# Kernel optimization log

Measured on AMD Instinct MI355X. Metric: run time of the kernel, lower is better.

Reference implementation:

```python
import jax, jax.numpy as jnp
import numpy as np

B, SQ, SK = 8, 2048, 2048
QE = KE = VE = HID = 1024
NORM = HID ** 0.5


def setup_inputs() -> dict:
    key0 = jax.random.key(0)
    ks = jax.random.split(key0, 9)
    s = 1.0 / np.sqrt(HID)
    return {
        "key": jax.random.normal(ks[0], (B, SK, KE), dtype=jnp.float32),
        "query": jax.random.normal(ks[1], (B, SQ, QE), dtype=jnp.float32),
        "mask": jax.random.randint(ks[2], (B, SQ, SK), 0, 2, dtype=jnp.int32),
        # nn.Linear params: W has shape [out, in], y = x @ W.T + b
        "Wq": jax.random.uniform(ks[3], (HID, QE), jnp.float32, -s, s),
        "bq": jax.random.uniform(ks[4], (HID,), jnp.float32, -s, s),
        "Wk": jax.random.uniform(ks[5], (HID, KE), jnp.float32, -s, s),
        "bk": jax.random.uniform(ks[6], (HID,), jnp.float32, -s, s),
        "Wv": jax.random.uniform(ks[7], (HID, VE), jnp.float32, -s, s),
        "bv": jax.random.uniform(ks[8], (HID,), jnp.float32, -s, s),
    }


def reference(key, query, mask, Wq, bq, Wk, bk, Wv, bv):
    # QKV projections (note: value projection is applied to `key`, as in the original)
    q = jnp.einsum('bse,he->bsh', query, Wq) + bq   # [B,SQ,H]
    k = jnp.einsum('bse,he->bsh', key, Wk) + bk     # [B,SK,H]
    v = jnp.einsum('bse,he->bsh', key, Wv) + bv     # [B,SK,H]
    # scores + mask (0 -> -inf) in one fused pass
    score = jnp.einsum('bqh,bkh->bqk', q, k) / NORM  # [B,SQ,SK]
    score = jnp.where(mask == 0, -jnp.inf, score)
    score = jax.nn.softmax(score, axis=-1)
    # NaN cleanup for fully-masked rows (score.data[score != score] = 0)
    score = jnp.where(jnp.isnan(score), 0.0, score)
    output = jnp.einsum('bqk,bkh->bqh', score, v)    # [B,SQ,H]
    return (output, score)
```

## Files before the change

### kernel.cpp

```cpp
#include <hip/hip_runtime.h>
#include <hip/hip_bf16.h>

typedef __bf16 bf16;
typedef __bf16 bf16x8 __attribute__((ext_vector_type(8)));
typedef float  f32x4  __attribute__((ext_vector_type(4)));
typedef int    i32x4  __attribute__((ext_vector_type(4)));

#define TM 128
#define TN 128
#define TK 32
#define LDS_PAD 40

typedef __attribute__((address_space(3))) void       lds_t;
typedef __attribute__((address_space(1))) const void gbl_t;
__device__ __forceinline__ void async16(const void* g, void* l) {
    __builtin_amdgcn_global_load_lds((gbl_t*)g, (lds_t*)l, 16, 0, 0);
}

template<typename TC, int BIAS, int NTC>
__global__ __launch_bounds__(256)
void gemm_bt(const bf16* __restrict__ A, const bf16* __restrict__ B,
             TC* __restrict__ C, const float* __restrict__ bias,
             int K, int lda, int ldb, int ldc,
             long sA, long sB, long sC)
{
    constexpr int ASZ = TM * TK;
    constexpr int BSZ = TN * TK;
    constexpr int BUF = ASZ + BSZ;
    __shared__ bf16 lds[3 * BUF];

    const int gx = gridDim.x, gy = gridDim.y;
    int lin = blockIdx.x + gx * (blockIdx.y + gy * blockIdx.z);
    const int cpx = (gx * gy * gridDim.z) >> 3;
    lin = (lin & 7) * cpx + (lin >> 3);
    const int bx  = lin % gx;
    const int rem = lin / gx;
    const int by  = rem % gy;
    const int bz  = rem / gy;

    A += (long)bz * sA;  B += (long)bz * sB;  C += (long)bz * sC;

    const int m0 = by * TM;
    const int n0 = bx * TN;

    const int t    = threadIdx.x;
    const int lane = t & 63;
    const int wave = t >> 6;
    const int wm   = (wave >> 1) * 64;
    const int wn   = (wave & 1) * 64;
    const int lrow = lane & 15;
    const int quad = lane >> 4;

    const int srow = lane >> 2;
    const int scol = (lane & 3) * 8;

    const bf16* pA = &A[(long)(m0 + wave * 16 + srow) * lda + scol];
    const bf16* pB = &B[(long)(n0 + wave * 16 + srow) * ldb + scol];
    const long jA = (long)64 * lda;
    const long jB = (long)64 * ldb;

    const int NT_ = K / TK;

    auto stage = [&](int tile, int oS) {
        const int k0 = tile * TK;
        #pragma unroll
        for (int j = 0; j < 2; ++j) {
            const int rg = j * 64 + wave * 16;
            async16(pA + j * jA + k0, &lds[oS + rg * TK]);
            async16(pB + j * jB + k0, &lds[oS + ASZ + rg * TK]);
        }
    };

    stage(0, 0);
    asm volatile("" ::: "memory");
    stage(1, BUF);

    int oC = 0, oN = BUF, oS = 2 * BUF;
    f32x4 acc[4][4] = {};

    for (int tt = 0; tt < NT_; ++tt) {
        if (tt < NT_ - 1) asm volatile("s_waitcnt vmcnt(4) lgkmcnt(0)" ::: "memory");
        else              asm volatile("s_waitcnt vmcnt(0) lgkmcnt(0)" ::: "memory");
        __builtin_amdgcn_s_barrier();
        __builtin_amdgcn_sched_barrier(0);

        if (tt + 2 < NT_) stage(tt + 2, oS);

        bf16x8 af[4], bfr[4];
        #pragma unroll
        for (int i = 0; i < 4; ++i)
            af[i] = *(bf16x8*)&lds[oC + (wm + i * 16 + lrow) * TK + quad * 8];
        #pragma unroll
        for (int j = 0; j < 4; ++j)
            bfr[j] = *(bf16x8*)&lds[oC + ASZ + (wn + j * 16 + lrow) * TK + quad * 8];

        #pragma unroll
        for (int i = 0; i < 4; ++i)
            #pragma unroll
            for (int j = 0; j < 4; ++j)
                acc[i][j] = __builtin_amdgcn_mfma_f32_16x16x32_bf16(
                    af[i], bfr[j], acc[i][j], 0, 0, 0);

        const int tmp = oC; oC = oN; oN = oS; oS = tmp;
    }

    #pragma unroll
    for (int i = 0; i < 4; ++i) {
        #pragma unroll
        for (int j = 0; j < 4; ++j) {
            #pragma unroll
            for (int r = 0; r < 4; ++r) {
                const int row = m0 + wm + i * 16 + quad * 4 + r;
                const int col = n0 + wn + j * 16 + lrow;
                float v = acc[i][j][r];
                if (BIAS == 1) v += bias[col];
                if (BIAS == 2) v += bias[row];
                if constexpr (NTC)
                    __builtin_nontemporal_store((TC)v, &C[(long)row * ldc + col]);
                else
                    C[(long)row * ldc + col] = (TC)v;
            }
        }
    }
}

__global__ __launch_bounds__(256)
void cvt_f32_bf16(const float* __restrict__ x, bf16* __restrict__ y)
{
    const long i = ((long)blockIdx.x * 256 + threadIdx.x) * 8;
    const f32x4 a = __builtin_nontemporal_load((const f32x4*)(x + i));
    const f32x4 b = __builtin_nontemporal_load((const f32x4*)(x + i + 4));
    bf16x8 v;
    v[0] = (bf16)a[0]; v[1] = (bf16)a[1]; v[2] = (bf16)a[2]; v[3] = (bf16)a[3];
    v[4] = (bf16)b[0]; v[5] = (bf16)b[1]; v[6] = (bf16)b[2]; v[7] = (bf16)b[3];
    *(bf16x8*)(y + i) = v;
}

template<typename T>
__device__ inline void stage8(bf16* dst, const T* src) {
    if constexpr (sizeof(T) == 4) {
        const float4 f0 = *(const float4*)src;
        const float4 f1 = *(const float4*)(src + 4);
        bf16x8 v;
        v[0] = (bf16)f0.x; v[1] = (bf16)f0.y; v[2] = (bf16)f0.z; v[3] = (bf16)f0.w;
        v[4] = (bf16)f1.x; v[5] = (bf16)f1.y; v[6] = (bf16)f1.z; v[7] = (bf16)f1.w;
        *(bf16x8*)dst = v;
    } else {
        *(uint4*)dst = *(const uint4*)src;
    }
}

template<typename TA, typename TB, typename TC, int BIAS>
__global__ __launch_bounds__(256)
void gemm_nt(const TA* __restrict__ A, const TB* __restrict__ B,
             TC* __restrict__ C, const float* __restrict__ bias,
             int K, int lda, int ldb, int ldc,
             long sA, long sB, long sC)
{
    __shared__ bf16 lsA[TM * LDS_PAD];
    __shared__ bf16 lsB[TN * LDS_PAD];

    const int bz = blockIdx.z;
    A += (long)bz * sA;  B += (long)bz * sB;  C += (long)bz * sC;

    const int m0 = blockIdx.y * TM;
    const int n0 = blockIdx.x * TN;

    const int t    = threadIdx.x;
    const int lane = t & 63;
    const int wave = t >> 6;
    const int wm   = (wave >> 1) * 64;
    const int wn   = (wave & 1) * 64;
    const int lrow = lane & 15;
    const int quad = lane >> 4;
    const int sr = t >> 2;
    const int sk = (t & 3) * 8;

    f32x4 acc[4][4] = {};

    for (int k0 = 0; k0 < K; k0 += TK) {
        __syncthreads();
        #pragma unroll
        for (int h = 0; h < 2; ++h) {
            const int row = h * 64 + sr;
            stage8(&lsA[row * LDS_PAD + sk], &A[(long)(m0 + row) * lda + k0 + sk]);
            stage8(&lsB[row * LDS_PAD + sk], &B[(long)(n0 + row) * ldb + k0 + sk]);
        }
        __syncthreads();

        bf16x8 af[4], bfr[4];
        #pragma unroll
        for (int i = 0; i < 4; ++i)
            af[i] = *(bf16x8*)&lsA[(wm + i * 16 + lrow) * LDS_PAD + quad * 8];
        #pragma unroll
        for (int j = 0; j < 4; ++j)
            bfr[j] = *(bf16x8*)&lsB[(wn + j * 16 + lrow) * LDS_PAD + quad * 8];

        #pragma unroll
        for (int i = 0; i < 4; ++i)
            #pragma unroll
            for (int j = 0; j < 4; ++j)
                acc[i][j] = __builtin_amdgcn_mfma_f32_16x16x32_bf16(
                    af[i], bfr[j], acc[i][j], 0, 0, 0);
    }

    #pragma unroll
    for (int i = 0; i < 4; ++i) {
        #pragma unroll
        for (int j = 0; j < 4; ++j) {
            #pragma unroll
            for (int r = 0; r < 4; ++r) {
                const int row = m0 + wm + i * 16 + quad * 4 + r;
                const int col = n0 + wn + j * 16 + lrow;
                float v = acc[i][j][r];
                if (BIAS == 1) v += bias[col];
                if (BIAS == 2) v += bias[row];
                C[(long)row * ldc + col] = (TC)v;
            }
        }
    }
}

template<int DUAL>
__global__ __launch_bounds__(256)
void softmax_rows(float* __restrict__ score, const int* __restrict__ mask,
                  bf16* __restrict__ pb)
{
    const int t = threadIdx.x;
    const long base = (long)blockIdx.x * 2048 + t * 8;

    const f32x4 a0 = __builtin_nontemporal_load((const f32x4*)(score + base));
    const f32x4 a1 = __builtin_nontemporal_load((const f32x4*)(score + base + 4));
    const i32x4 mA = __builtin_nontemporal_load((const i32x4*)(mask + base));
    const i32x4 mB = __builtin_nontemporal_load((const i32x4*)(mask + base + 4));

    const float INV = 0.03125f;
    float s[8];
    #pragma unroll
    for (int i = 0; i < 4; ++i) s[i]     = mA[i] ? a0[i] * INV : -INFINITY;
    #pragma unroll
    for (int i = 0; i < 4; ++i) s[4 + i] = mB[i] ? a1[i] * INV : -INFINITY;

    float mx = s[0];
    #pragma unroll
    for (int i = 1; i < 8; ++i) mx = fmaxf(mx, s[i]);
    #pragma unroll
    for (int o = 32; o > 0; o >>= 1) mx = fmaxf(mx, __shfl_xor(mx, o, 64));

    __shared__ float redm[4], reds[4];
    const int wave = t >> 6, lane = t & 63;
    if (lane == 0) redm[wave] = mx;
    __syncthreads();
    mx = fmaxf(fmaxf(redm[0], redm[1]), fmaxf(redm[2], redm[3]));

    const bool dead = !(mx > -INFINITY);
    float e[8], sum = 0.f;
    #pragma unroll
    for (int i = 0; i < 8; ++i) {
        const float x = dead ? 0.0f : __expf(s[i] - mx);
        e[i] = x;
        sum += x;
    }
    #pragma unroll
    for (int o = 32; o > 0; o >>= 1) sum += __shfl_xor(sum, o, 64);
    if (lane == 0) reds[wave] = sum;
    __syncthreads();
    sum = reds[0] + reds[1] + reds[2] + reds[3];

    const float inv = dead ? 0.0f : (1.0f / sum);
    f32x4 o0, o1;
    float p[8];
    #pragma unroll
    for (int i = 0; i < 8; ++i) p[i] = e[i] * inv;
    o0[0] = p[0]; o0[1] = p[1]; o0[2] = p[2]; o0[3] = p[3];
    o1[0] = p[4]; o1[1] = p[5]; o1[2] = p[6]; o1[3] = p[7];

    __builtin_nontemporal_store(o0, (f32x4*)(score + base));
    __builtin_nontemporal_store(o1, (f32x4*)(score + base + 4));
    if (DUAL) {
        bf16x8 v;
        #pragma unroll
        for (int i = 0; i < 8; ++i) v[i] = (bf16)p[i];
        *(bf16x8*)(pb + base) = v;
    }
}

extern "C" void kernel_launch(void* const* d_in, const int* in_sizes, int n_in,
                              void* d_out, int out_size, void* d_ws, size_t ws_size,
                              hipStream_t stream)
{
    const float* key   = (const float*)d_in[0];
    const float* query = (const float*)d_in[1];
    const int*   mask  = (const int*)d_in[2];
    const float* Wq = (const float*)d_in[3];
    const float* bq = (const float*)d_in[4];
    const float* Wk = (const float*)d_in[5];
    const float* bk = (const float*)d_in[6];
    const float* Wv = (const float*)d_in[7];
    const float* bv = (const float*)d_in[8];

    float* out   = (float*)d_out;
    float* score = out + (size_t)8 * 2048 * 1024;

    const dim3 blk(256, 1, 1);
    const long SB = (long)2048 * 1024;
    const long SS = (long)2048 * 2048;
    const size_t NX = (size_t)8 * 2048 * 1024;
    const size_t NW = (size_t)1024 * 1024;

    const size_t NEED = (4 * NX + 3 * NW) * sizeof(bf16);

    if (ws_size >= NEED) {
        bf16* xb = (bf16*)d_ws;
        bf16* qb = xb + NX;
        bf16* kb = qb + NX;
        bf16* vt = kb + NX;
        bf16* wq = vt + NX;
        bf16* wk = wq + NW;
        bf16* wv = wk + NW;
        bf16* Pb = xb;

        cvt_f32_bf16<<<dim3(NW / 2048), blk, 0, stream>>>(Wq, wq);
        cvt_f32_bf16<<<dim3(NW / 2048), blk, 0, stream>>>(Wk, wk);
        cvt_f32_bf16<<<dim3(NW / 2048), blk, 0, stream>>>(Wv, wv);

        cvt_f32_bf16<<<dim3(NX / 2048), blk, 0, stream>>>(key, xb);
        gemm_bt<bf16, 1, 0><<<dim3(8, 128, 1), blk, 0, stream>>>(
            xb, wk, kb, bk, 1024, 1024, 1024, 1024, 0, 0, 0);
        gemm_bt<bf16, 2, 0><<<dim3(16, 8, 8), blk, 0, stream>>>(
            wv, xb, vt, bv, 1024, 1024, 1024, 2048, 0, SB, SB);

        cvt_f32_bf16<<<dim3(NX / 2048), blk, 0, stream>>>(query, xb);
        gemm_bt<bf16, 1, 0><<<dim3(8, 128, 1), blk, 0, stream>>>(
            xb, wq, qb, bq, 1024, 1024, 1024, 1024, 0, 0, 0);

        gemm_bt<float, 0, 1><<<dim3(16, 16, 8), blk, 0, stream>>>(
            qb, kb, score, nullptr, 1024, 1024, 1024, 2048, SB, SB, SS);

        softmax_rows<1><<<dim3(16384), blk, 0, stream>>>(score, mask, Pb);

        gemm_bt<float, 0, 1><<<dim3(8, 16, 8), blk, 0, stream>>>(
            Pb, vt, out, nullptr, 2048, 2048, 2048, 1024, SS, SB, SB);
    } else {
        bf16* qb = (bf16*)d_ws;
        bf16* kb = qb + NX;
        bf16* vt = kb + NX;

        gemm_nt<float, float, bf16, 1><<<dim3(8, 128, 1), blk, 0, stream>>>(
            query, Wq, qb, bq, 1024, 1024, 1024, 1024, 0, 0, 0);
        gemm_nt<float, float, bf16, 1><<<dim3(8, 128, 1), blk, 0, stream>>>(
            key, Wk, kb, bk, 1024, 1024, 1024, 1024, 0, 0, 0);
        gemm_nt<float, float, bf16, 2><<<dim3(16, 8, 8), blk, 0, stream>>>(
            Wv, key, vt, bv, 1024, 1024, 1024, 2048, 0, SB, SB);
        gemm_nt<bf16, bf16, float, 0><<<dim3(16, 16, 8), blk, 0, stream>>>(
            qb, kb, score, nullptr, 1024, 1024, 1024, 2048, SB, SB, SS);
        softmax_rows<0><<<dim3(16384), blk, 0, stream>>>(score, mask, nullptr);
        gemm_nt<float, bf16, float, 0><<<dim3(8, 16, 8), blk, 0, stream>>>(
            score, vt, out, nullptr, 2048, 2048, 2048, 1024, SS, SB, SB);
    }
}
```

Before: 686.8 us.

## Enlarge gemm_bt block tile to 256x128 and cache score between GEMM and softmax

The pipelined bf16 GEMM moves from a 128x128 to a 256x128 output tile per block. Each wave now computes 128x64 with an 8x4 accumulator array, so there are more MFMAs per LDS B-fragment and fewer blocks, and the grids are halved to match. Launch bounds request two blocks per CU. The score store is switched from nontemporal to normal stores and softmax loads it with plain loads, so the 128MB score buffer may partly stay in cache between the two kernels. The larger tile raises register and LDS pressure and halves the number of blocks, which could hurt occupancy.

```diff
diff --git a/kernel.cpp b/kernel.cpp
--- a/kernel.cpp
+++ b/kernel.cpp
@@ -6,9 +6,9 @@
 typedef float  f32x4  __attribute__((ext_vector_type(4)));
 typedef int    i32x4  __attribute__((ext_vector_type(4)));
 
-#define TM 128
-#define TN 128
 #define TK 32
+#define FB_TM 128
+#define FB_TN 128
 #define LDS_PAD 40
 
 typedef __attribute__((address_space(3))) void       lds_t;
@@ -18,16 +18,17 @@
 }
 
 template<typename TC, int BIAS, int NTC>
-__global__ __launch_bounds__(256)
+__global__ __launch_bounds__(256, 2)
 void gemm_bt(const bf16* __restrict__ A, const bf16* __restrict__ B,
              TC* __restrict__ C, const float* __restrict__ bias,
              int K, int lda, int ldb, int ldc,
              long sA, long sB, long sC)
 {
-    constexpr int ASZ = TM * TK;
-    constexpr int BSZ = TN * TK;
-    constexpr int BUF = ASZ + BSZ;
-    __shared__ bf16 lds[3 * BUF];
+    constexpr int BM  = 256, BN = 128;
+    constexpr int ASZ = BM * TK;
+    constexpr int BSZ = BN * TK;
+    constexpr int BUFE = ASZ + BSZ;
+    __shared__ bf16 lds[3 * BUFE];
 
     const int gx = gridDim.x, gy = gridDim.y;
     int lin = blockIdx.x + gx * (blockIdx.y + gy * blockIdx.z);
@@ -40,13 +41,13 @@
 
     A += (long)bz * sA;  B += (long)bz * sB;  C += (long)bz * sC;
 
-    const int m0 = by * TM;
-    const int n0 = bx * TN;
+    const int m0 = by * BM;
+    const int n0 = bx * BN;
 
     const int t    = threadIdx.x;
     const int lane = t & 63;
     const int wave = t >> 6;
-    const int wm   = (wave >> 1) * 64;
+    const int wm   = (wave >> 1) * 128;
     const int wn   = (wave & 1) * 64;
     const int lrow = lane & 15;
     const int quad = lane >> 4;
@@ -56,46 +57,46 @@
 
     const bf16* pA = &A[(long)(m0 + wave * 16 + srow) * lda + scol];
     const bf16* pB = &B[(long)(n0 + wave * 16 + srow) * ldb + scol];
-    const long jA = (long)64 * lda;
-    const long jB = (long)64 * ldb;
 
     const int NT_ = K / TK;
 
     auto stage = [&](int tile, int oS) {
         const int k0 = tile * TK;
         #pragma unroll
-        for (int j = 0; j < 2; ++j) {
-            const int rg = j * 64 + wave * 16;
-            async16(pA + j * jA + k0, &lds[oS + rg * TK]);
-            async16(pB + j * jB + k0, &lds[oS + ASZ + rg * TK]);
-        }
+        for (int j = 0; j < 4; ++j)
+            async16(pA + (long)(j * 64) * lda + k0,
+                    &lds[oS + (wave * 16 + j * 64) * TK]);
+        #pragma unroll
+        for (int j = 0; j < 2; ++j)
+            async16(pB + (long)(j * 64) * ldb + k0,
+                    &lds[oS + ASZ + (wave * 16 + j * 64) * TK]);
     };
 
     stage(0, 0);
     asm volatile("" ::: "memory");
-    stage(1, BUF);
-
-    int oC = 0, oN = BUF, oS = 2 * BUF;
-    f32x4 acc[4][4] = {};
+    stage(1, BUFE);
+
+    int oC = 0, oN = BUFE, oS = 2 * BUFE;
+    f32x4 acc[8][4] = {};
 
     for (int tt = 0; tt < NT_; ++tt) {
-        if (tt < NT_ - 1) asm volatile("s_waitcnt vmcnt(4) lgkmcnt(0)" ::: "memory");
+        if (tt < NT_ - 1) asm volatile("s_waitcnt vmcnt(6) lgkmcnt(0)" ::: "memory");
         else              asm volatile("s_waitcnt vmcnt(0) lgkmcnt(0)" ::: "memory");
         __builtin_amdgcn_s_barrier();
         __builtin_amdgcn_sched_barrier(0);
 
         if (tt + 2 < NT_) stage(tt + 2, oS);
 
-        bf16x8 af[4], bfr[4];
-        #pragma unroll
-        for (int i = 0; i < 4; ++i)
+        bf16x8 af[8], bfr[4];
+        #pragma unroll
+        for (int i = 0; i < 8; ++i)
             af[i] = *(bf16x8*)&lds[oC + (wm + i * 16 + lrow) * TK + quad * 8];
         #pragma unroll
         for (int j = 0; j < 4; ++j)
             bfr[j] = *(bf16x8*)&lds[oC + ASZ + (wn + j * 16 + lrow) * TK + quad * 8];
 
         #pragma unroll
-        for (int i = 0; i < 4; ++i)
+        for (int i = 0; i < 8; ++i)
             #pragma unroll
             for (int j = 0; j < 4; ++j)
                 acc[i][j] = __builtin_amdgcn_mfma_f32_16x16x32_bf16(
@@ -105,7 +106,7 @@
     }
 
     #pragma unroll
-    for (int i = 0; i < 4; ++i) {
+    for (int i = 0; i < 8; ++i) {
         #pragma unroll
         for (int j = 0; j < 4; ++j) {
             #pragma unroll
@@ -157,14 +158,14 @@
              int K, int lda, int ldb, int ldc,
              long sA, long sB, long sC)
 {
-    __shared__ bf16 lsA[TM * LDS_PAD];
-    __shared__ bf16 lsB[TN * LDS_PAD];
+    __shared__ bf16 lsA[FB_TM * LDS_PAD];
+    __shared__ bf16 lsB[FB_TN * LDS_PAD];
 
     const int bz = blockIdx.z;
     A += (long)bz * sA;  B += (long)bz * sB;  C += (long)bz * sC;
 
-    const int m0 = blockIdx.y * TM;
-    const int n0 = blockIdx.x * TN;
+    const int m0 = blockIdx.y * FB_TM;
+    const int n0 = blockIdx.x * FB_TN;
 
     const int t    = threadIdx.x;
     const int lane = t & 63;
@@ -229,8 +230,8 @@
     const int t = threadIdx.x;
     const long base = (long)blockIdx.x * 2048 + t * 8;
 
-    const f32x4 a0 = __builtin_nontemporal_load((const f32x4*)(score + base));
-    const f32x4 a1 = __builtin_nontemporal_load((const f32x4*)(score + base + 4));
+    const f32x4 a0 = *(const f32x4*)(score + base);
+    const f32x4 a1 = *(const f32x4*)(score + base + 4);
     const i32x4 mA = __builtin_nontemporal_load((const i32x4*)(mask + base));
     const i32x4 mB = __builtin_nontemporal_load((const i32x4*)(mask + base + 4));
 
@@ -325,21 +326,21 @@
         cvt_f32_bf16<<<dim3(NW / 2048), blk, 0, stream>>>(Wv, wv);
 
         cvt_f32_bf16<<<dim3(NX / 2048), blk, 0, stream>>>(key, xb);
-        gemm_bt<bf16, 1, 0><<<dim3(8, 128, 1), blk, 0, stream>>>(
+        gemm_bt<bf16, 1, 0><<<dim3(8, 64, 1), blk, 0, stream>>>(
             xb, wk, kb, bk, 1024, 1024, 1024, 1024, 0, 0, 0);
-        gemm_bt<bf16, 2, 0><<<dim3(16, 8, 8), blk, 0, stream>>>(
+        gemm_bt<bf16, 2, 0><<<dim3(16, 4, 8), blk, 0, stream>>>(
             wv, xb, vt, bv, 1024, 1024, 1024, 2048, 0, SB, SB);
 
         cvt_f32_bf16<<<dim3(NX / 2048), blk, 0, stream>>>(query, xb);
-        gemm_bt<bf16, 1, 0><<<dim3(8, 128, 1), blk, 0, stream>>>(
+        gemm_bt<bf16, 1, 0><<<dim3(8, 64, 1), blk, 0, stream>>>(
             xb, wq, qb, bq, 1024, 1024, 1024, 1024, 0, 0, 0);
 
-        gemm_bt<float, 0, 1><<<dim3(16, 16, 8), blk, 0, stream>>>(
+        gemm_bt<float, 0, 0><<<dim3(16, 8, 8), blk, 0, stream>>>(
             qb, kb, score, nullptr, 1024, 1024, 1024, 2048, SB, SB, SS);
 
         softmax_rows<1><<<dim3(16384), blk, 0, stream>>>(score, mask, Pb);
 
-        gemm_bt<float, 0, 1><<<dim3(8, 16, 8), blk, 0, stream>>>(
+        gemm_bt<float, 0, 1><<<dim3(8, 8, 8), blk, 0, stream>>>(
             Pb, vt, out, nullptr, 2048, 2048, 2048, 1024, SS, SB, SB);
     } else {
         bf16* qb = (bf16*)d_ws;
```

New measurement: 653.8 us. -4.8%, faster.
